# Kernel tuning notes

Hardware: AMD Instinct MI355X
Metric: run time of the kernel (lower is better)

Reference implementation:

```python
import jax, jax.numpy as jnp
import numpy as np

N = 50000
E = 1600000
IN_CH = 128
OUT_CH = 128
NEG_SLOPE = 0.2


def _gat_conv(x, W, att_src, att_dst, bias, src, dst, heads, out_ch, concat):
    # x: [N, F_in], W: [F_in, heads*out_ch], att_*: [heads, out_ch]
    n = x.shape[0]
    h = (x @ W).reshape(n, heads, out_ch)                    # [N, H, C]
    a_src = jnp.einsum('nhc,hc->nh', h, att_src)             # [N, H]
    a_dst = jnp.einsum('nhc,hc->nh', h, att_dst)             # [N, H]
    logits = jax.nn.leaky_relu(a_src[src] + a_dst[dst], NEG_SLOPE)  # [Etot, H]
    m = jax.ops.segment_max(logits, dst, num_segments=n)     # per-dst max (self-loops ensure non-empty)
    e = jnp.exp(logits - m[dst])
    denom = jax.ops.segment_sum(e, dst, num_segments=n)
    alpha = e / denom[dst]                                   # [Etot, H]
    msgs = h[src] * alpha[:, :, None]                        # [Etot, H, C]
    out = jax.ops.segment_sum(msgs, dst, num_segments=n)     # [N, H, C]
    out = out.reshape(n, heads * out_ch) if concat else out.mean(axis=1)
    return out + bias


def setup_inputs() -> dict:
    key = jax.random.key(0)
    ks = jax.random.split(key, 12)
    x = jax.random.normal(ks[0], (N, IN_CH), dtype=jnp.float32)
    edge_index = jax.random.randint(ks[1], (2, E), 0, N, dtype=jnp.int32)
    s = 0.1
    W_map = jax.random.normal(ks[2], (IN_CH, OUT_CH), dtype=jnp.float32) * s
    b_map = jnp.zeros((OUT_CH,), dtype=jnp.float32)
    # conv1: 128 -> 8 per head, 8 heads
    W1 = jax.random.normal(ks[3], (OUT_CH, 64), dtype=jnp.float32) * s
    att_src1 = jax.random.normal(ks[4], (8, 8), dtype=jnp.float32) * s
    att_dst1 = jax.random.normal(ks[5], (8, 8), dtype=jnp.float32) * s
    b1 = jnp.zeros((64,), dtype=jnp.float32)
    # conv2: 64 -> 128, 1 head, concat=False
    W2 = jax.random.normal(ks[6], (64, OUT_CH), dtype=jnp.float32) * s
    att_src2 = jax.random.normal(ks[7], (1, OUT_CH), dtype=jnp.float32) * s
    att_dst2 = jax.random.normal(ks[8], (1, OUT_CH), dtype=jnp.float32) * s
    b2 = jnp.zeros((OUT_CH,), dtype=jnp.float32)
    return {"x": x, "edge_index": edge_index, "W_map": W_map, "b_map": b_map,
            "W1": W1, "att_src1": att_src1, "att_dst1": att_dst1, "b1": b1,
            "W2": W2, "att_src2": att_src2, "att_dst2": att_dst2, "b2": b2}


def reference(x, edge_index, W_map, b_map, W1, att_src1, att_dst1, b1,
              W2, att_src2, att_dst2, b2):
    # add self-loops (PyG GATConv default)
    loops = jnp.arange(N, dtype=edge_index.dtype)
    src = jnp.concatenate([edge_index[0], loops])
    dst = jnp.concatenate([edge_index[1], loops])
    h = x @ W_map + b_map                                   # feature_mapping (dropout inactive in eval)
    h = _gat_conv(h, W1, att_src1, att_dst1, b1, src, dst, heads=8, out_ch=8, concat=True)
    h = jax.nn.elu(h)
    out = _gat_conv(h, W2, att_src2, att_dst2, b2, src, dst, heads=1, out_ch=OUT_CH, concat=False)
    return out
```

## Files before the change

### kernel.cpp

```cpp
#include <hip/hip_runtime.h>
#include <cstdint>
#include <cstddef>

#define NEG_SLOPE 0.2f
#define NBIN_MAX 1024
#define CAP_T 2560
#define SC_BLOCKS 512

typedef __attribute__((ext_vector_type(8))) short bf16x8;
typedef __attribute__((ext_vector_type(4))) float f32x4;

__device__ __forceinline__ float leaky(float x) { return x > 0.f ? x : NEG_SLOPE * x; }
__device__ __forceinline__ float blo(unsigned u) { return __uint_as_float(u << 16); }
__device__ __forceinline__ float bhi(unsigned u) { return __uint_as_float(u & 0xffff0000u); }
__device__ __forceinline__ unsigned short f2b(float f) {
    unsigned b = __float_as_uint(f);
    return (unsigned short)((b + 0x7fffu + ((b >> 16) & 1u)) >> 16);
}

__global__ void prep_kernel(const float* __restrict__ Wm, const float* __restrict__ W1,
                            const float* __restrict__ bm, const float* __restrict__ W2,
                            unsigned short* __restrict__ WcT, float* __restrict__ bc,
                            unsigned short* __restrict__ W2T, int* __restrict__ ccur,
                            int nbin) {
    int t = blockIdx.x * 256 + threadIdx.x;
    if (t < nbin) ccur[t] = 0;
    if (t < 8192) {
        int n = t >> 7, k = t & 127;
        float acc = 0.f;
        for (int c = 0; c < 128; c++) acc = fmaf(Wm[k * 128 + c], W1[c * 64 + n], acc);
        WcT[n * 128 + k] = f2b(acc);
        if (t < 64) {
            float a = 0.f;
            for (int c = 0; c < 128; c++) a = fmaf(bm[c], W1[c * 64 + t], a);
            bc[t] = a;
        }
    } else if (t < 16384) {
        int u = t - 8192;
        int n = u >> 6, k = u & 63;
        W2T[n * 64 + k] = f2b(W2[k * 128 + n]);
    }
}

__global__ __launch_bounds__(256) void phase2_kernel(
    const int* __restrict__ src, const int* __restrict__ dst, int E, int nbin,
    int* __restrict__ ccur, unsigned* __restrict__ tmp,
    const float* __restrict__ x, const unsigned short* __restrict__ WcT,
    const float* __restrict__ bc, const float* __restrict__ att_s,
    const float* __restrict__ att_d, unsigned short* __restrict__ h1b,
    float* __restrict__ as1, float* __restrict__ ad1, int N) {
    __shared__ int cnt[NBIN_MAX];
    if (blockIdx.x < SC_BLOCKS) {
        for (int i = threadIdx.x; i < nbin; i += 256) cnt[i] = 0;
        __syncthreads();
        int E4 = E >> 2;
        int chunk4 = (E4 + SC_BLOCKS - 1) / SC_BLOCKS;
        int b4 = blockIdx.x * chunk4;
        int e4 = b4 + chunk4; if (e4 > E4) e4 = E4;
        const int4* dst4 = (const int4*)dst;
        const int4* src4 = (const int4*)src;
        bool last = (blockIdx.x == SC_BLOCKS - 1);
        for (int i = b4 + threadIdx.x; i < e4; i += 256) {
            int4 d = dst4[i];
            atomicAdd(&cnt[d.x >> 6], 1);
            atomicAdd(&cnt[d.y >> 6], 1);
            atomicAdd(&cnt[d.z >> 6], 1);
            atomicAdd(&cnt[d.w >> 6], 1);
        }
        if (last)
            for (int i = (E4 << 2) + threadIdx.x; i < E; i += 256)
                atomicAdd(&cnt[dst[i] >> 6], 1);
        __syncthreads();
        for (int i = threadIdx.x; i < nbin; i += 256) {
            int c = cnt[i];
            cnt[i] = c ? atomicAdd(&ccur[i], c) : 0;
        }
        __syncthreads();
        for (int i = b4 + threadIdx.x; i < e4; i += 256) {
            int4 d = dst4[i];
            int4 s = src4[i];
#pragma unroll
            for (int k = 0; k < 4; k++) {
                int dd = (k == 0) ? d.x : (k == 1) ? d.y : (k == 2) ? d.z : d.w;
                int ss = (k == 0) ? s.x : (k == 1) ? s.y : (k == 2) ? s.z : s.w;
                int bin = dd >> 6;
                int p = atomicAdd(&cnt[bin], 1);
                if (p < CAP_T)
                    tmp[(size_t)bin * CAP_T + p] = ((unsigned)ss << 6) | (unsigned)(dd & 63);
            }
        }
        if (last)
            for (int i = (E4 << 2) + threadIdx.x; i < E; i += 256) {
                int dd = dst[i];
                int bin = dd >> 6;
                int p = atomicAdd(&cnt[bin], 1);
                if (p < CAP_T)
                    tmp[(size_t)bin * CAP_T + p] = ((unsigned)src[i] << 6) | (unsigned)(dd & 63);
            }
        return;
    }
    int wave = threadIdx.x >> 6, l = threadIdx.x & 63;
    int mtile = (blockIdx.x - SC_BLOCKS) * 4 + wave;
    int mtiles = N >> 4;
    if (mtile >= mtiles) return;
    int lm = l & 15, quad = l >> 4;
    const float* xr = x + ((size_t)(mtile * 16 + lm)) * 128 + quad * 8;
    f32x4 acc[4];
#pragma unroll
    for (int nt = 0; nt < 4; nt++) acc[nt] = (f32x4){0.f, 0.f, 0.f, 0.f};
#pragma unroll
    for (int kk = 0; kk < 4; kk++) {
        float4 xa = ((const float4*)(xr + kk * 32))[0];
        float4 xb = ((const float4*)(xr + kk * 32 + 4))[0];
        bf16x8 a;
        a[0] = (short)f2b(xa.x); a[1] = (short)f2b(xa.y);
        a[2] = (short)f2b(xa.z); a[3] = (short)f2b(xa.w);
        a[4] = (short)f2b(xb.x); a[5] = (short)f2b(xb.y);
        a[6] = (short)f2b(xb.z); a[7] = (short)f2b(xb.w);
#pragma unroll
        for (int nt = 0; nt < 4; nt++) {
            bf16x8 b = *(const bf16x8*)(WcT + (nt * 16 + lm) * 128 + kk * 32 + quad * 8);
            acc[nt] = __builtin_amdgcn_mfma_f32_16x16x32_bf16(a, b, acc[nt], 0, 0, 0);
        }
    }
    float vs[4][4], vd[4][4];
#pragma unroll
    for (int nt = 0; nt < 4; nt++) {
        int col = nt * 16 + lm;
        float sA = att_s[col], dA = att_d[col], bcv = bc[col];
#pragma unroll
        for (int r = 0; r < 4; r++) {
            float hv = acc[nt][r] + bcv;
            int row = mtile * 16 + quad * 4 + r;
            h1b[(size_t)row * 64 + col] = f2b(hv);
            vs[nt][r] = hv * sA;
            vd[nt][r] = hv * dA;
        }
    }
#pragma unroll
    for (int m = 1; m < 8; m <<= 1)
#pragma unroll
        for (int nt = 0; nt < 4; nt++)
#pragma unroll
            for (int r = 0; r < 4; r++) {
                vs[nt][r] += __shfl_xor(vs[nt][r], m);
                vd[nt][r] += __shfl_xor(vd[nt][r], m);
            }
    if ((lm & 7) == 0) {
        int hbase = lm >> 3;
#pragma unroll
        for (int nt = 0; nt < 4; nt++) {
            int H = 2 * nt + hbase;
#pragma unroll
            for (int r = 0; r < 4; r++) {
                int row = mtile * 16 + quad * 4 + r;
                as1[row * 8 + H] = vs[nt][r];
                ad1[row * 8 + H] = vd[nt][r];
            }
        }
    }
}

__global__ __launch_bounds__(256) void bin_finalize(
    const unsigned* __restrict__ tmp, const int* __restrict__ ccur,
    int* __restrict__ off, int* __restrict__ degv,
    unsigned short* __restrict__ bucket, int N) {
    __shared__ int cnt[64];
    __shared__ int cur[64];
    __shared__ unsigned short lbkt[CAP_T];
    int tid = threadIdx.x, b = blockIdx.x;
    if (tid < 64) cnt[tid] = 0;
    __syncthreads();
    int ecnt = ccur[b]; if (ecnt > CAP_T) ecnt = CAP_T;
    const unsigned* t = tmp + (size_t)b * CAP_T;
    const uint4* t4 = (const uint4*)t;
    int e4 = ecnt >> 2;
    for (int i = tid; i < e4; i += 256) {
        uint4 v = t4[i];
        atomicAdd(&cnt[v.x & 63u], 1);
        atomicAdd(&cnt[v.y & 63u], 1);
        atomicAdd(&cnt[v.z & 63u], 1);
        atomicAdd(&cnt[v.w & 63u], 1);
    }
    for (int i = (e4 << 2) + tid; i < ecnt; i += 256)
        atomicAdd(&cnt[t[i] & 63u], 1);
    __syncthreads();
    if (tid < 64) {
        int v = cnt[tid];
        int incl = v;
#pragma unroll
        for (int s = 1; s < 64; s <<= 1) {
            int u = __shfl_up(incl, s);
            if (tid >= s) incl += u;
        }
        int excl = incl - v;
        int node = b * 64 + tid;
        if (node < N) { off[node] = b * CAP_T + excl; degv[node] = v; }
        cur[tid] = excl;
    }
    __syncthreads();
    for (int i = tid; i < e4; i += 256) {
        uint4 v = t4[i];
        int p0 = atomicAdd(&cur[v.x & 63u], 1); lbkt[p0] = (unsigned short)(v.x >> 6);
        int p1 = atomicAdd(&cur[v.y & 63u], 1); lbkt[p1] = (unsigned short)(v.y >> 6);
        int p2 = atomicAdd(&cur[v.z & 63u], 1); lbkt[p2] = (unsigned short)(v.z >> 6);
        int p3 = atomicAdd(&cur[v.w & 63u], 1); lbkt[p3] = (unsigned short)(v.w >> 6);
    }
    for (int i = (e4 << 2) + tid; i < ecnt; i += 256) {
        unsigned u = t[i];
        int p = atomicAdd(&cur[u & 63u], 1);
        lbkt[p] = (unsigned short)(u >> 6);
    }
    __syncthreads();
    unsigned short* db = bucket + (size_t)b * CAP_T;
    int e8 = ecnt >> 3;
    uint4* d4 = (uint4*)db;
    const uint4* l4 = (const uint4*)lbkt;
    for (int i = tid; i < e8; i += 256) d4[i] = l4[i];
    for (int i = (e8 << 3) + tid; i < ecnt; i += 256) db[i] = lbkt[i];
}

__global__ __launch_bounds__(256) void conv1_agg(
    const int* __restrict__ off, const int* __restrict__ degv,
    const unsigned short* __restrict__ bucket,
    const unsigned* __restrict__ h1b, const float* __restrict__ as1,
    const float* __restrict__ ad1, const float* __restrict__ b1,
    unsigned* __restrict__ h1act, int N) {
    __shared__ uint2 lw[4][32][8];
    int wave = threadIdx.x >> 6, l = threadIdx.x & 63;
    int n = blockIdx.x * 4 + wave;
    if (n >= N) return;
    int begin = off[n];
    int deg = degv[n];
    int h = l & 7, eslot = l >> 3;
    float adst_h = ad1[n * 8 + h];
    float wself_h = __expf(leaky(as1[n * 8 + h] + adst_h));
    int c = l & 31, hp = c >> 2, half = l >> 5;
    float wself_c = __shfl(wself_h, hp);
    float acc0 = 0.f, acc1 = 0.f;
    if (half == 0) {
        unsigned u = h1b[(size_t)n * 32 + c];
        acc0 = wself_c * blo(u);
        acc1 = wself_c * bhi(u);
    }
    float den_l = 0.f;
    unsigned ps[4]; float pa[4];
#pragma unroll
    for (int k = 0; k < 4; k++) {
        int j = eslot + 8 * k;
        ps[k] = (j < deg) ? (unsigned)bucket[begin + j] : 0u;
    }
#pragma unroll
    for (int k = 0; k < 4; k++) pa[k] = as1[ps[k] * 8 + h];
    for (int c0 = 0; c0 < deg; c0 += 32) {
#pragma unroll
        for (int k = 0; k < 4; k++) {
            int e = eslot + 8 * k;
            float w = __expf(leaky(pa[k] + adst_h));
            if (c0 + e >= deg) w = 0.f;
            den_l += w;
            lw[wave][e][h] = make_uint2(__float_as_uint(w), ps[k]);
        }
        int c1 = c0 + 32;
        if (c1 < deg) {
#pragma unroll
            for (int k = 0; k < 4; k++) {
                int j = c1 + eslot + 8 * k;
                ps[k] = (j < deg) ? (unsigned)bucket[begin + j] : 0u;
            }
#pragma unroll
            for (int k = 0; k < 4; k++) pa[k] = as1[ps[k] * 8 + h];
        }
        int cend = deg - c0; if (cend > 32) cend = 32;
        int e = half;
        for (; e + 14 < cend; e += 16) {
            float w[8]; unsigned s[8], u[8];
#pragma unroll
            for (int k = 0; k < 8; k++) {
                uint2 p = lw[wave][e + 2 * k][hp];
                w[k] = __uint_as_float(p.x); s[k] = p.y;
            }
#pragma unroll
            for (int k = 0; k < 8; k++) u[k] = h1b[(size_t)s[k] * 32 + c];
#pragma unroll
            for (int k = 0; k < 8; k++) {
                acc0 = fmaf(w[k], blo(u[k]), acc0);
                acc1 = fmaf(w[k], bhi(u[k]), acc1);
            }
        }
        for (; e < cend; e += 2) {
            uint2 p = lw[wave][e][hp];
            unsigned u = h1b[(size_t)p.y * 32 + c];
            float w = __uint_as_float(p.x);
            acc0 = fmaf(w, blo(u), acc0);
            acc1 = fmaf(w, bhi(u), acc1);
        }
    }
    den_l += __shfl_xor(den_l, 8);
    den_l += __shfl_xor(den_l, 16);
    den_l += __shfl_xor(den_l, 32);
    float den_full = den_l + wself_h;
    float den_c = __shfl(den_full, hp);
    acc0 += __shfl_xor(acc0, 32);
    acc1 += __shfl_xor(acc1, 32);
    if (half == 0) {
        float inv = 1.f / den_c;
        float2 bb = ((const float2*)b1)[c];
        float o0 = acc0 * inv + bb.x;
        float o1 = acc1 * inv + bb.y;
        o0 = o0 > 0.f ? o0 : __expf(o0) - 1.f;
        o1 = o1 > 0.f ? o1 : __expf(o1) - 1.f;
        h1act[(size_t)n * 32 + c] = (unsigned)f2b(o0) | ((unsigned)f2b(o1) << 16);
    }
}

__global__ __launch_bounds__(256) void gemm2_mfma(
    const unsigned short* __restrict__ h1act, const unsigned short* __restrict__ W2T,
    const float* __restrict__ att_s2, const float* __restrict__ att_d2,
    unsigned short* __restrict__ h2b, float* __restrict__ as2, float* __restrict__ ad2,
    int N) {
    int wave = threadIdx.x >> 6, l = threadIdx.x & 63;
    int mtile = blockIdx.x * 4 + wave;
    int mtiles = N >> 4;
    if (mtile >= mtiles) return;
    int lm = l & 15, quad = l >> 4;
    const unsigned short* ar = h1act + (size_t)(mtile * 16 + lm) * 64 + quad * 8;
    bf16x8 a0 = *(const bf16x8*)(ar);
    bf16x8 a1 = *(const bf16x8*)(ar + 32);
    f32x4 acc[8];
#pragma unroll
    for (int nt = 0; nt < 8; nt++) acc[nt] = (f32x4){0.f, 0.f, 0.f, 0.f};
#pragma unroll
    for (int nt = 0; nt < 8; nt++) {
        const unsigned short* br = W2T + (nt * 16 + lm) * 64 + quad * 8;
        bf16x8 b0 = *(const bf16x8*)(br);
        bf16x8 b1v = *(const bf16x8*)(br + 32);
        acc[nt] = __builtin_amdgcn_mfma_f32_16x16x32_bf16(a0, b0, acc[nt], 0, 0, 0);
        acc[nt] = __builtin_amdgcn_mfma_f32_16x16x32_bf16(a1, b1v, acc[nt], 0, 0, 0);
    }
    float vs[4] = {0.f, 0.f, 0.f, 0.f}, vd[4] = {0.f, 0.f, 0.f, 0.f};
#pragma unroll
    for (int nt = 0; nt < 8; nt++) {
        int col = nt * 16 + lm;
        float sA = att_s2[col], dA = att_d2[col];
#pragma unroll
        for (int r = 0; r < 4; r++) {
            float hv = acc[nt][r];
            int row = mtile * 16 + quad * 4 + r;
            h2b[(size_t)row * 128 + col] = f2b(hv);
            vs[r] = fmaf(hv, sA, vs[r]);
            vd[r] = fmaf(hv, dA, vd[r]);
        }
    }
#pragma unroll
    for (int m = 1; m < 16; m <<= 1)
#pragma unroll
        for (int r = 0; r < 4; r++) {
            vs[r] += __shfl_xor(vs[r], m);
            vd[r] += __shfl_xor(vd[r], m);
        }
    if (lm == 0) {
#pragma unroll
        for (int r = 0; r < 4; r++) {
            int row = mtile * 16 + quad * 4 + r;
            as2[row] = vs[r];
            ad2[row] = vd[r];
        }
    }
}

__global__ __launch_bounds__(256) void conv2_agg(
    const int* __restrict__ off, const int* __restrict__ degv,
    const unsigned short* __restrict__ bucket,
    const unsigned* __restrict__ h2b, const float* __restrict__ as2,
    const float* __restrict__ ad2, const float* __restrict__ b2,
    float* __restrict__ out, int N) {
    __shared__ uint2 ew[4][64];
    int wave = threadIdx.x >> 6, l = threadIdx.x & 63;
    int n = blockIdx.x * 4 + wave;
    if (n >= N) return;
    int begin = off[n];
    int deg = degv[n];
    float adst = ad2[n];
    float wself = __expf(leaky(as2[n] + adst));
    unsigned us = h2b[(size_t)n * 64 + l];
    float acc0 = wself * blo(us);
    float acc1 = wself * bhi(us);
    float den_l = 0.f;
    for (int c0 = 0; c0 < deg; c0 += 64) {
        int j = c0 + l;
        float w = 0.f; unsigned s = 0;
        if (j < deg) {
            s = bucket[begin + j];
            w = __expf(leaky(as2[s] + adst));
        }
        den_l += w;
        ew[wave][l] = make_uint2(__float_as_uint(w), s);
        int cend = deg - c0; if (cend > 64) cend = 64;
        int jj = 0;
        for (; jj + 8 <= cend; jj += 8) {
            float w[8]; unsigned s8[8], u[8];
#pragma unroll
            for (int k = 0; k < 8; k++) {
                uint2 p = ew[wave][jj + k];
                w[k] = __uint_as_float(p.x); s8[k] = p.y;
            }
#pragma unroll
            for (int k = 0; k < 8; k++) u[k] = h2b[(size_t)s8[k] * 64 + l];
#pragma unroll
            for (int k = 0; k < 8; k++) {
                acc0 = fmaf(w[k], blo(u[k]), acc0);
                acc1 = fmaf(w[k], bhi(u[k]), acc1);
            }
        }
        for (; jj < cend; jj++) {
            uint2 p0 = ew[wave][jj];
            unsigned u0 = h2b[(size_t)p0.y * 64 + l];
            float w0 = __uint_as_float(p0.x);
            acc0 = fmaf(w0, blo(u0), acc0); acc1 = fmaf(w0, bhi(u0), acc1);
        }
    }
#pragma unroll
    for (int s = 1; s < 64; s <<= 1) den_l += __shfl_xor(den_l, s);
    float inv = 1.f / (den_l + wself);
    float2 bb = ((const float2*)b2)[l];
    ((float2*)out)[(size_t)n * 64 + l] =
        make_float2(acc0 * inv + bb.x, acc1 * inv + bb.y);
}

extern "C" void kernel_launch(void* const* d_in, const int* in_sizes, int n_in,
                              void* d_out, int out_size, void* d_ws, size_t ws_size,
                              hipStream_t stream) {
    const float* x   = (const float*)d_in[0];
    const int*   ei  = (const int*)d_in[1];
    const float* Wm  = (const float*)d_in[2];
    const float* bm  = (const float*)d_in[3];
    const float* W1  = (const float*)d_in[4];
    const float* As1 = (const float*)d_in[5];
    const float* Ad1 = (const float*)d_in[6];
    const float* b1  = (const float*)d_in[7];
    const float* W2  = (const float*)d_in[8];
    const float* As2 = (const float*)d_in[9];
    const float* Ad2 = (const float*)d_in[10];
    const float* b2  = (const float*)d_in[11];
    int N = in_sizes[0] / 128;
    int E = in_sizes[1] / 2;
    const int* srcv = ei;
    const int* dstv = ei + E;

    char* p = (char*)d_ws;
    auto alloc = [&](size_t bytes) {
        void* r = (void*)p;
        p += (bytes + 255) & ~(size_t)255;
        return r;
    };
    int nbin = (N + 63) / 64;
    int*   degv   = (int*)alloc((size_t)N * 4);
    int*   off    = (int*)alloc((size_t)N * 4);
    int*   ccur   = (int*)alloc((size_t)nbin * 4);
    unsigned short* bucket = (unsigned short*)alloc((size_t)nbin * CAP_T * 2);
    unsigned short* WcT  = (unsigned short*)alloc(64 * 128 * 2);
    float*          bc   = (float*)alloc(64 * 4);
    unsigned short* W2T  = (unsigned short*)alloc(128 * 64 * 2);
    unsigned short* h1b  = (unsigned short*)alloc((size_t)N * 64 * 2);
    float* a_s1   = (float*)alloc((size_t)N * 8 * 4);
    float* a_d1   = (float*)alloc((size_t)N * 8 * 4);
    unsigned* h1act = (unsigned*)alloc((size_t)N * 64 * 2);
    unsigned short* h2b = (unsigned short*)alloc((size_t)N * 128 * 2);
    unsigned* tmp = (unsigned*)h2b;
    float* a_s2   = (float*)alloc((size_t)N * 4);
    float* a_d2   = (float*)alloc((size_t)N * 4);
    float* outp   = (float*)d_out;

    int mtiles = N >> 4;
    int gemm_blocks = (mtiles + 3) / 4;
    prep_kernel<<<64, 256, 0, stream>>>(Wm, W1, bm, W2, WcT, bc, W2T, ccur, nbin);
    phase2_kernel<<<SC_BLOCKS + gemm_blocks, 256, 0, stream>>>(
        srcv, dstv, E, nbin, ccur, tmp, x, WcT, bc, As1, Ad1, h1b, a_s1, a_d1, N);
    bin_finalize<<<nbin, 256, 0, stream>>>(tmp, ccur, off, degv, bucket, N);
    conv1_agg<<<(N + 3) / 4, 256, 0, stream>>>(off, degv, bucket, (const unsigned*)h1b, a_s1, a_d1, b1, h1act, N);
    gemm2_mfma<<<(mtiles + 3) / 4, 256, 0, stream>>>((const unsigned short*)h1act, W2T, As2, Ad2, h2b, a_s2, a_d2, N);
    conv2_agg<<<(N + 3) / 4, 256, 0, stream>>>(off, degv, bucket, (const unsigned*)h2b, a_s2, a_d2, b2, outp, N);
}
```

Measured before the change: 270.5 us.

## Widen gathers to 8-byte loads and software-pipeline edge batches in both aggregations

Both aggregation kernels now gather 8 bytes per lane (four bf16 features) instead of 4, so each wave processes 4 (conv1) or 2 (conv2) edges at once. Edge chunks grow to 64 for conv1, and the inner loop is software-pipelined: the next batch of 8 gathers is issued before the current batch's FMAs. Neighbour offsets are pre-shifted into byte offsets in shared memory, and the shared array is padded to 9 columns to avoid bank conflicts. The unrolled full batches process padded zero-weight edges, which costs extra FMAs and loads for low-degree nodes, and the extra in-flight loads raise register pressure.

```diff
diff --git a/kernel.cpp b/kernel.cpp
--- a/kernel.cpp
+++ b/kernel.cpp
@@ -226,91 +226,115 @@
     const unsigned* __restrict__ h1b, const float* __restrict__ as1,
     const float* __restrict__ ad1, const float* __restrict__ b1,
     unsigned* __restrict__ h1act, int N) {
-    __shared__ uint2 lw[4][32][8];
+    __shared__ uint2 lw[4][64][9];
     int wave = threadIdx.x >> 6, l = threadIdx.x & 63;
     int n = blockIdx.x * 4 + wave;
     if (n >= N) return;
     int begin = off[n];
     int deg = degv[n];
     int h = l & 7, eslot = l >> 3;
+    int qq = l & 15, quarter = l >> 4, hh = qq >> 1;
+    unsigned qoff = (unsigned)(qq << 3);
+    const char* h1c = (const char*)h1b;
     float adst_h = ad1[n * 8 + h];
     float wself_h = __expf(leaky(as1[n * 8 + h] + adst_h));
-    int c = l & 31, hp = c >> 2, half = l >> 5;
-    float wself_c = __shfl(wself_h, hp);
-    float acc0 = 0.f, acc1 = 0.f;
-    if (half == 0) {
-        unsigned u = h1b[(size_t)n * 32 + c];
-        acc0 = wself_c * blo(u);
-        acc1 = wself_c * bhi(u);
+    float wself_c = __shfl(wself_h, hh);
+    float acc[4] = {0.f, 0.f, 0.f, 0.f};
+    if (quarter == 0) {
+        uint2 us = *(const uint2*)(h1c + ((unsigned)n << 7) + qoff);
+        acc[0] = wself_c * blo(us.x);
+        acc[1] = wself_c * bhi(us.x);
+        acc[2] = wself_c * blo(us.y);
+        acc[3] = wself_c * bhi(us.y);
     }
     float den_l = 0.f;
-    unsigned ps[4]; float pa[4];
-#pragma unroll
-    for (int k = 0; k < 4; k++) {
+    unsigned ps[8]; float pa[8];
+#pragma unroll
+    for (int k = 0; k < 8; k++) {
         int j = eslot + 8 * k;
         ps[k] = (j < deg) ? (unsigned)bucket[begin + j] : 0u;
     }
 #pragma unroll
-    for (int k = 0; k < 4; k++) pa[k] = as1[ps[k] * 8 + h];
-    for (int c0 = 0; c0 < deg; c0 += 32) {
-#pragma unroll
-        for (int k = 0; k < 4; k++) {
+    for (int k = 0; k < 8; k++) pa[k] = as1[ps[k] * 8 + h];
+    for (int c0 = 0; c0 < deg; c0 += 64) {
+#pragma unroll
+        for (int k = 0; k < 8; k++) {
             int e = eslot + 8 * k;
             float w = __expf(leaky(pa[k] + adst_h));
             if (c0 + e >= deg) w = 0.f;
             den_l += w;
-            lw[wave][e][h] = make_uint2(__float_as_uint(w), ps[k]);
-        }
-        int c1 = c0 + 32;
+            lw[wave][e][h] = make_uint2(__float_as_uint(w), ps[k] << 7);
+        }
+        int c1 = c0 + 64;
         if (c1 < deg) {
 #pragma unroll
-            for (int k = 0; k < 4; k++) {
+            for (int k = 0; k < 8; k++) {
                 int j = c1 + eslot + 8 * k;
                 ps[k] = (j < deg) ? (unsigned)bucket[begin + j] : 0u;
             }
 #pragma unroll
-            for (int k = 0; k < 4; k++) pa[k] = as1[ps[k] * 8 + h];
-        }
-        int cend = deg - c0; if (cend > 32) cend = 32;
-        int e = half;
-        for (; e + 14 < cend; e += 16) {
-            float w[8]; unsigned s[8], u[8];
+            for (int k = 0; k < 8; k++) pa[k] = as1[ps[k] * 8 + h];
+        }
+        int cend = deg - c0; if (cend > 64) cend = 64;
+        int K = (cend + 3) >> 2;
+        int nb = (K + 7) >> 3;
+        float wv[8]; uint2 u[8];
+#pragma unroll
+        for (int k = 0; k < 8; k++) {
+            uint2 p = lw[wave][4 * k + quarter][hh];
+            wv[k] = __uint_as_float(p.x);
+            u[k] = *(const uint2*)(h1c + p.y + qoff);
+        }
+        for (int b = 1; b < nb; b++) {
+            float wn[8]; uint2 un[8];
 #pragma unroll
             for (int k = 0; k < 8; k++) {
-                uint2 p = lw[wave][e + 2 * k][hp];
-                w[k] = __uint_as_float(p.x); s[k] = p.y;
-            }
-#pragma unroll
-            for (int k = 0; k < 8; k++) u[k] = h1b[(size_t)s[k] * 32 + c];
+                uint2 p = lw[wave][((b << 3) + k) * 4 + quarter][hh];
+                wn[k] = __uint_as_float(p.x);
+                un[k] = *(const uint2*)(h1c + p.y + qoff);
+            }
 #pragma unroll
             for (int k = 0; k < 8; k++) {
-                acc0 = fmaf(w[k], blo(u[k]), acc0);
-                acc1 = fmaf(w[k], bhi(u[k]), acc1);
-            }
-        }
-        for (; e < cend; e += 2) {
-            uint2 p = lw[wave][e][hp];
-            unsigned u = h1b[(size_t)p.y * 32 + c];
-            float w = __uint_as_float(p.x);
-            acc0 = fmaf(w, blo(u), acc0);
-            acc1 = fmaf(w, bhi(u), acc1);
+                acc[0] = fmaf(wv[k], blo(u[k].x), acc[0]);
+                acc[1] = fmaf(wv[k], bhi(u[k].x), acc[1]);
+                acc[2] = fmaf(wv[k], blo(u[k].y), acc[2]);
+                acc[3] = fmaf(wv[k], bhi(u[k].y), acc[3]);
+            }
+#pragma unroll
+            for (int k = 0; k < 8; k++) { wv[k] = wn[k]; u[k] = un[k]; }
+        }
+#pragma unroll
+        for (int k = 0; k < 8; k++) {
+            acc[0] = fmaf(wv[k], blo(u[k].x), acc[0]);
+            acc[1] = fmaf(wv[k], bhi(u[k].x), acc[1]);
+            acc[2] = fmaf(wv[k], blo(u[k].y), acc[2]);
+            acc[3] = fmaf(wv[k], bhi(u[k].y), acc[3]);
         }
     }
     den_l += __shfl_xor(den_l, 8);
     den_l += __shfl_xor(den_l, 16);
     den_l += __shfl_xor(den_l, 32);
     float den_full = den_l + wself_h;
-    float den_c = __shfl(den_full, hp);
-    acc0 += __shfl_xor(acc0, 32);
-    acc1 += __shfl_xor(acc1, 32);
-    if (half == 0) {
+    float den_c = __shfl(den_full, hh);
+#pragma unroll
+    for (int i = 0; i < 4; i++) {
+        acc[i] += __shfl_xor(acc[i], 16);
+        acc[i] += __shfl_xor(acc[i], 32);
+    }
+    if (quarter == 0) {
         float inv = 1.f / den_c;
-        float2 bb = ((const float2*)b1)[c];
-        float o0 = acc0 * inv + bb.x;
-        float o1 = acc1 * inv + bb.y;
+        float4 bb = ((const float4*)b1)[qq];
+        float o0 = acc[0] * inv + bb.x;
+        float o1 = acc[1] * inv + bb.y;
+        float o2 = acc[2] * inv + bb.z;
+        float o3 = acc[3] * inv + bb.w;
         o0 = o0 > 0.f ? o0 : __expf(o0) - 1.f;
         o1 = o1 > 0.f ? o1 : __expf(o1) - 1.f;
-        h1act[(size_t)n * 32 + c] = (unsigned)f2b(o0) | ((unsigned)f2b(o1) << 16);
+        o2 = o2 > 0.f ? o2 : __expf(o2) - 1.f;
+        o3 = o3 > 0.f ? o3 : __expf(o3) - 1.f;
+        ((uint2*)h1act)[(size_t)n * 16 + qq] = make_uint2(
+            (unsigned)f2b(o0) | ((unsigned)f2b(o1) << 16),
+            (unsigned)f2b(o2) | ((unsigned)f2b(o3) << 16));
     }
 }
 
@@ -381,51 +405,77 @@
     if (n >= N) return;
     int begin = off[n];
     int deg = degv[n];
+    int half = l >> 5, q = l & 31;
+    unsigned qoff = (unsigned)(q << 3);
+    const char* h2c = (const char*)h2b;
     float adst = ad2[n];
     float wself = __expf(leaky(as2[n] + adst));
-    unsigned us = h2b[(size_t)n * 64 + l];
-    float acc0 = wself * blo(us);
-    float acc1 = wself * bhi(us);
+    float acc[4] = {0.f, 0.f, 0.f, 0.f};
+    if (half == 0) {
+        uint2 us = *(const uint2*)(h2c + ((unsigned)n << 8) + qoff);
+        acc[0] = wself * blo(us.x);
+        acc[1] = wself * bhi(us.x);
+        acc[2] = wself * blo(us.y);
+        acc[3] = wself * bhi(us.y);
+    }
     float den_l = 0.f;
     for (int c0 = 0; c0 < deg; c0 += 64) {
         int j = c0 + l;
-        float w = 0.f; unsigned s = 0;
+        float w = 0.f; unsigned soff = 0u;
         if (j < deg) {
-            s = bucket[begin + j];
+            unsigned s = (unsigned)bucket[begin + j];
+            soff = s << 8;
             w = __expf(leaky(as2[s] + adst));
         }
         den_l += w;
-        ew[wave][l] = make_uint2(__float_as_uint(w), s);
+        ew[wave][l] = make_uint2(__float_as_uint(w), soff);
         int cend = deg - c0; if (cend > 64) cend = 64;
-        int jj = 0;
-        for (; jj + 8 <= cend; jj += 8) {
-            float w[8]; unsigned s8[8], u[8];
+        int K = (cend + 1) >> 1;
+        int nb = (K + 7) >> 3;
+        float wv[8]; uint2 u[8];
+#pragma unroll
+        for (int k = 0; k < 8; k++) {
+            uint2 p = ew[wave][2 * k + half];
+            wv[k] = __uint_as_float(p.x);
+            u[k] = *(const uint2*)(h2c + p.y + qoff);
+        }
+        for (int b = 1; b < nb; b++) {
+            float wn[8]; uint2 un[8];
 #pragma unroll
             for (int k = 0; k < 8; k++) {
-                uint2 p = ew[wave][jj + k];
-                w[k] = __uint_as_float(p.x); s8[k] = p.y;
-            }
-#pragma unroll
-            for (int k = 0; k < 8; k++) u[k] = h2b[(size_t)s8[k] * 64 + l];
+                uint2 p = ew[wave][((b << 3) + k) * 2 + half];
+                wn[k] = __uint_as_float(p.x);
+                un[k] = *(const uint2*)(h2c + p.y + qoff);
+            }
 #pragma unroll
             for (int k = 0; k < 8; k++) {
-                acc0 = fmaf(w[k], blo(u[k]), acc0);
-                acc1 = fmaf(w[k], bhi(u[k]), acc1);
-            }
-        }
-        for (; jj < cend; jj++) {
-            uint2 p0 = ew[wave][jj];
-            unsigned u0 = h2b[(size_t)p0.y * 64 + l];
-            float w0 = __uint_as_float(p0.x);
-            acc0 = fmaf(w0, blo(u0), acc0); acc1 = fmaf(w0, bhi(u0), acc1);
+                acc[0] = fmaf(wv[k], blo(u[k].x), acc[0]);
+                acc[1] = fmaf(wv[k], bhi(u[k].x), acc[1]);
+                acc[2] = fmaf(wv[k], blo(u[k].y), acc[2]);
+                acc[3] = fmaf(wv[k], bhi(u[k].y), acc[3]);
+            }
+#pragma unroll
+            for (int k = 0; k < 8; k++) { wv[k] = wn[k]; u[k] = un[k]; }
+        }
+#pragma unroll
+        for (int k = 0; k < 8; k++) {
+            acc[0] = fmaf(wv[k], blo(u[k].x), acc[0]);
+            acc[1] = fmaf(wv[k], bhi(u[k].x), acc[1]);
+            acc[2] = fmaf(wv[k], blo(u[k].y), acc[2]);
+            acc[3] = fmaf(wv[k], bhi(u[k].y), acc[3]);
         }
     }
 #pragma unroll
     for (int s = 1; s < 64; s <<= 1) den_l += __shfl_xor(den_l, s);
     float inv = 1.f / (den_l + wself);
-    float2 bb = ((const float2*)b2)[l];
-    ((float2*)out)[(size_t)n * 64 + l] =
-        make_float2(acc0 * inv + bb.x, acc1 * inv + bb.y);
+#pragma unroll
+    for (int i = 0; i < 4; i++) acc[i] += __shfl_xor(acc[i], 32);
+    if (half == 0) {
+        float4 bb = ((const float4*)b2)[q];
+        ((float4*)out)[(size_t)n * 32 + q] = make_float4(
+            acc[0] * inv + bb.x, acc[1] * inv + bb.y,
+            acc[2] * inv + bb.z, acc[3] * inv + bb.w);
+    }
 }
 
 extern "C" void kernel_launch(void* const* d_in, const int* in_sizes, int n_in,
```

Measured after the change: 293.7 us. +8.6%, slower.

## Gather neighbor rows with 16-byte vector loads in both GAT aggregation kernels

Applied to the files above, without the earlier changes.

Both aggregation kernels now have each lane own 8 contiguous bf16 channels and gather them with a single 16-byte load per edge. The wave processes several edges at once, and per-edge weights are computed in registers. Neighbor indices and attention scores are prefetched one chunk ahead, which removes the shared-memory weight/index staging. The goal is fewer, wider gather instructions and more memory-level parallelism. The cost is more registers and a cross-lane reduction of 8 accumulators at the end.

```diff
diff --git a/kernel.cpp b/kernel.cpp
--- a/kernel.cpp
+++ b/kernel.cpp
@@ -226,91 +226,115 @@
     const unsigned* __restrict__ h1b, const float* __restrict__ as1,
     const float* __restrict__ ad1, const float* __restrict__ b1,
     unsigned* __restrict__ h1act, int N) {
-    __shared__ uint2 lw[4][32][8];
     int wave = threadIdx.x >> 6, l = threadIdx.x & 63;
     int n = blockIdx.x * 4 + wave;
     if (n >= N) return;
     int begin = off[n];
     int deg = degv[n];
-    int h = l & 7, eslot = l >> 3;
-    float adst_h = ad1[n * 8 + h];
-    float wself_h = __expf(leaky(as1[n * 8 + h] + adst_h));
-    int c = l & 31, hp = c >> 2, half = l >> 5;
-    float wself_c = __shfl(wself_h, hp);
-    float acc0 = 0.f, acc1 = 0.f;
-    if (half == 0) {
-        unsigned u = h1b[(size_t)n * 32 + c];
-        acc0 = wself_c * blo(u);
-        acc1 = wself_c * bhi(u);
+    int oo = l & 7, octet = l >> 3;
+    unsigned qoff = (unsigned)(oo << 4);
+    const char* h1c = (const char*)h1b;
+    float adst = ad1[n * 8 + oo];
+    float wself = __expf(leaky(as1[n * 8 + oo] + adst));
+    float acc[8] = {0.f, 0.f, 0.f, 0.f, 0.f, 0.f, 0.f, 0.f};
+    if (octet == 0) {
+        uint4 us = *(const uint4*)(h1c + ((size_t)n << 7) + qoff);
+        acc[0] = wself * blo(us.x); acc[1] = wself * bhi(us.x);
+        acc[2] = wself * blo(us.y); acc[3] = wself * bhi(us.y);
+        acc[4] = wself * blo(us.z); acc[5] = wself * bhi(us.z);
+        acc[6] = wself * blo(us.w); acc[7] = wself * bhi(us.w);
     }
     float den_l = 0.f;
-    unsigned ps[4]; float pa[4];
-#pragma unroll
-    for (int k = 0; k < 4; k++) {
-        int j = eslot + 8 * k;
-        ps[k] = (j < deg) ? (unsigned)bucket[begin + j] : 0u;
-    }
-#pragma unroll
-    for (int k = 0; k < 4; k++) pa[k] = as1[ps[k] * 8 + h];
-    for (int c0 = 0; c0 < deg; c0 += 32) {
-#pragma unroll
-        for (int k = 0; k < 4; k++) {
-            int e = eslot + 8 * k;
-            float w = __expf(leaky(pa[k] + adst_h));
-            if (c0 + e >= deg) w = 0.f;
-            den_l += w;
-            lw[wave][e][h] = make_uint2(__float_as_uint(w), ps[k]);
-        }
-        int c1 = c0 + 32;
-        if (c1 < deg) {
-#pragma unroll
-            for (int k = 0; k < 4; k++) {
-                int j = c1 + eslot + 8 * k;
-                ps[k] = (j < deg) ? (unsigned)bucket[begin + j] : 0u;
-            }
-#pragma unroll
-            for (int k = 0; k < 4; k++) pa[k] = as1[ps[k] * 8 + h];
-        }
-        int cend = deg - c0; if (cend > 32) cend = 32;
-        int e = half;
-        for (; e + 14 < cend; e += 16) {
-            float w[8]; unsigned s[8], u[8];
-#pragma unroll
-            for (int k = 0; k < 8; k++) {
-                uint2 p = lw[wave][e + 2 * k][hp];
-                w[k] = __uint_as_float(p.x); s[k] = p.y;
-            }
-#pragma unroll
-            for (int k = 0; k < 8; k++) u[k] = h1b[(size_t)s[k] * 32 + c];
-#pragma unroll
-            for (int k = 0; k < 8; k++) {
-                acc0 = fmaf(w[k], blo(u[k]), acc0);
-                acc1 = fmaf(w[k], bhi(u[k]), acc1);
-            }
-        }
-        for (; e < cend; e += 2) {
-            uint2 p = lw[wave][e][hp];
-            unsigned u = h1b[(size_t)p.y * 32 + c];
-            float w = __uint_as_float(p.x);
-            acc0 = fmaf(w, blo(u), acc0);
-            acc1 = fmaf(w, bhi(u), acc1);
+    unsigned sv[8]; float av[8];
+#pragma unroll
+    for (int j = 0; j < 8; j++) {
+        int e = 8 * j + octet;
+        sv[j] = (e < deg) ? (unsigned)bucket[begin + e] : 0u;
+    }
+#pragma unroll
+    for (int j = 0; j < 8; j++) {
+        float t = as1[sv[j] * 8 + oo];
+        av[j] = (8 * j + octet < deg) ? t : -1e30f;
+    }
+    for (int c0 = 0; c0 < deg; c0 += 64) {
+        uint4 uv[8];
+#pragma unroll
+        for (int j = 0; j < 8; j++) {
+            uv[j] = make_uint4(0u, 0u, 0u, 0u);
+            if (av[j] > -1e29f)
+                uv[j] = *(const uint4*)(h1c + ((size_t)sv[j] << 7) + qoff);
+        }
+        int c1 = c0 + 64;
+        bool more = c1 < deg;
+        unsigned sn[8];
+        if (more) {
+#pragma unroll
+            for (int j = 0; j < 8; j++) {
+                int e = c1 + 8 * j + octet;
+                sn[j] = (e < deg) ? (unsigned)bucket[begin + e] : 0u;
+            }
+        }
+        float wv[8];
+#pragma unroll
+        for (int j = 0; j < 8; j++) {
+            float w = __expf(leaky(av[j] + adst));
+            wv[j] = w; den_l += w;
+        }
+        if (more) {
+#pragma unroll
+            for (int j = 0; j < 8; j++) {
+                float t = as1[sn[j] * 8 + oo];
+                av[j] = (c1 + 8 * j + octet < deg) ? t : -1e30f;
+                sv[j] = sn[j];
+            }
+        }
+#pragma unroll
+        for (int j = 0; j < 8; j++) {
+            acc[0] = fmaf(wv[j], blo(uv[j].x), acc[0]);
+            acc[1] = fmaf(wv[j], bhi(uv[j].x), acc[1]);
+            acc[2] = fmaf(wv[j], blo(uv[j].y), acc[2]);
+            acc[3] = fmaf(wv[j], bhi(uv[j].y), acc[3]);
+            acc[4] = fmaf(wv[j], blo(uv[j].z), acc[4]);
+            acc[5] = fmaf(wv[j], bhi(uv[j].z), acc[5]);
+            acc[6] = fmaf(wv[j], blo(uv[j].w), acc[6]);
+            acc[7] = fmaf(wv[j], bhi(uv[j].w), acc[7]);
         }
     }
     den_l += __shfl_xor(den_l, 8);
     den_l += __shfl_xor(den_l, 16);
     den_l += __shfl_xor(den_l, 32);
-    float den_full = den_l + wself_h;
-    float den_c = __shfl(den_full, hp);
-    acc0 += __shfl_xor(acc0, 32);
-    acc1 += __shfl_xor(acc1, 32);
-    if (half == 0) {
-        float inv = 1.f / den_c;
-        float2 bb = ((const float2*)b1)[c];
-        float o0 = acc0 * inv + bb.x;
-        float o1 = acc1 * inv + bb.y;
+    float den = den_l + wself;
+#pragma unroll
+    for (int i = 0; i < 8; i++) {
+        acc[i] += __shfl_xor(acc[i], 8);
+        acc[i] += __shfl_xor(acc[i], 16);
+        acc[i] += __shfl_xor(acc[i], 32);
+    }
+    if (octet == 0) {
+        float inv = 1.f / den;
+        float4 b0 = ((const float4*)b1)[oo * 2];
+        float4 b1v = ((const float4*)b1)[oo * 2 + 1];
+        float o0 = acc[0] * inv + b0.x;
+        float o1 = acc[1] * inv + b0.y;
+        float o2 = acc[2] * inv + b0.z;
+        float o3 = acc[3] * inv + b0.w;
+        float o4 = acc[4] * inv + b1v.x;
+        float o5 = acc[5] * inv + b1v.y;
+        float o6 = acc[6] * inv + b1v.z;
+        float o7 = acc[7] * inv + b1v.w;
         o0 = o0 > 0.f ? o0 : __expf(o0) - 1.f;
         o1 = o1 > 0.f ? o1 : __expf(o1) - 1.f;
-        h1act[(size_t)n * 32 + c] = (unsigned)f2b(o0) | ((unsigned)f2b(o1) << 16);
+        o2 = o2 > 0.f ? o2 : __expf(o2) - 1.f;
+        o3 = o3 > 0.f ? o3 : __expf(o3) - 1.f;
+        o4 = o4 > 0.f ? o4 : __expf(o4) - 1.f;
+        o5 = o5 > 0.f ? o5 : __expf(o5) - 1.f;
+        o6 = o6 > 0.f ? o6 : __expf(o6) - 1.f;
+        o7 = o7 > 0.f ? o7 : __expf(o7) - 1.f;
+        unsigned r0 = (unsigned)f2b(o0) | ((unsigned)f2b(o1) << 16);
+        unsigned r1 = (unsigned)f2b(o2) | ((unsigned)f2b(o3) << 16);
+        unsigned r2 = (unsigned)f2b(o4) | ((unsigned)f2b(o5) << 16);
+        unsigned r3 = (unsigned)f2b(o6) | ((unsigned)f2b(o7) << 16);
+        ((uint4*)h1act)[(size_t)n * 8 + oo] = make_uint4(r0, r1, r2, r3);
     }
 }
 
@@ -375,57 +399,99 @@
     const unsigned* __restrict__ h2b, const float* __restrict__ as2,
     const float* __restrict__ ad2, const float* __restrict__ b2,
     float* __restrict__ out, int N) {
-    __shared__ uint2 ew[4][64];
     int wave = threadIdx.x >> 6, l = threadIdx.x & 63;
     int n = blockIdx.x * 4 + wave;
     if (n >= N) return;
     int begin = off[n];
     int deg = degv[n];
+    int qq = l & 15, quarter = l >> 4;
+    unsigned qoff = (unsigned)(qq << 4);
+    const char* h2c = (const char*)h2b;
     float adst = ad2[n];
     float wself = __expf(leaky(as2[n] + adst));
-    unsigned us = h2b[(size_t)n * 64 + l];
-    float acc0 = wself * blo(us);
-    float acc1 = wself * bhi(us);
+    float acc[8] = {0.f, 0.f, 0.f, 0.f, 0.f, 0.f, 0.f, 0.f};
+    if (quarter == 0) {
+        uint4 us = *(const uint4*)(h2c + ((size_t)n << 8) + qoff);
+        acc[0] = wself * blo(us.x); acc[1] = wself * bhi(us.x);
+        acc[2] = wself * blo(us.y); acc[3] = wself * bhi(us.y);
+        acc[4] = wself * blo(us.z); acc[5] = wself * bhi(us.z);
+        acc[6] = wself * blo(us.w); acc[7] = wself * bhi(us.w);
+    }
     float den_l = 0.f;
-    for (int c0 = 0; c0 < deg; c0 += 64) {
-        int j = c0 + l;
-        float w = 0.f; unsigned s = 0;
-        if (j < deg) {
-            s = bucket[begin + j];
-            w = __expf(leaky(as2[s] + adst));
-        }
-        den_l += w;
-        ew[wave][l] = make_uint2(__float_as_uint(w), s);
-        int cend = deg - c0; if (cend > 64) cend = 64;
-        int jj = 0;
-        for (; jj + 8 <= cend; jj += 8) {
-            float w[8]; unsigned s8[8], u[8];
-#pragma unroll
-            for (int k = 0; k < 8; k++) {
-                uint2 p = ew[wave][jj + k];
-                w[k] = __uint_as_float(p.x); s8[k] = p.y;
-            }
-#pragma unroll
-            for (int k = 0; k < 8; k++) u[k] = h2b[(size_t)s8[k] * 64 + l];
-#pragma unroll
-            for (int k = 0; k < 8; k++) {
-                acc0 = fmaf(w[k], blo(u[k]), acc0);
-                acc1 = fmaf(w[k], bhi(u[k]), acc1);
-            }
-        }
-        for (; jj < cend; jj++) {
-            uint2 p0 = ew[wave][jj];
-            unsigned u0 = h2b[(size_t)p0.y * 64 + l];
-            float w0 = __uint_as_float(p0.x);
-            acc0 = fmaf(w0, blo(u0), acc0); acc1 = fmaf(w0, bhi(u0), acc1);
-        }
-    }
-#pragma unroll
-    for (int s = 1; s < 64; s <<= 1) den_l += __shfl_xor(den_l, s);
-    float inv = 1.f / (den_l + wself);
-    float2 bb = ((const float2*)b2)[l];
-    ((float2*)out)[(size_t)n * 64 + l] =
-        make_float2(acc0 * inv + bb.x, acc1 * inv + bb.y);
+    unsigned sv[8]; float av[8];
+#pragma unroll
+    for (int j = 0; j < 8; j++) {
+        int e = 4 * j + quarter;
+        sv[j] = (e < deg) ? (unsigned)bucket[begin + e] : 0u;
+    }
+#pragma unroll
+    for (int j = 0; j < 8; j++) {
+        float t = as2[sv[j]];
+        av[j] = (4 * j + quarter < deg) ? t : -1e30f;
+    }
+    for (int c0 = 0; c0 < deg; c0 += 32) {
+        uint4 uv[8];
+#pragma unroll
+        for (int j = 0; j < 8; j++) {
+            uv[j] = make_uint4(0u, 0u, 0u, 0u);
+            if (av[j] > -1e29f)
+                uv[j] = *(const uint4*)(h2c + ((size_t)sv[j] << 8) + qoff);
+        }
+        int c1 = c0 + 32;
+        bool more = c1 < deg;
+        unsigned sn[8];
+        if (more) {
+#pragma unroll
+            for (int j = 0; j < 8; j++) {
+                int e = c1 + 4 * j + quarter;
+                sn[j] = (e < deg) ? (unsigned)bucket[begin + e] : 0u;
+            }
+        }
+        float wv[8];
+#pragma unroll
+        for (int j = 0; j < 8; j++) {
+            float w = __expf(leaky(av[j] + adst));
+            wv[j] = w; den_l += w;
+        }
+        if (more) {
+#pragma unroll
+            for (int j = 0; j < 8; j++) {
+                float t = as2[sn[j]];
+                av[j] = (c1 + 4 * j + quarter < deg) ? t : -1e30f;
+                sv[j] = sn[j];
+            }
+        }
+#pragma unroll
+        for (int j = 0; j < 8; j++) {
+            acc[0] = fmaf(wv[j], blo(uv[j].x), acc[0]);
+            acc[1] = fmaf(wv[j], bhi(uv[j].x), acc[1]);
+            acc[2] = fmaf(wv[j], blo(uv[j].y), acc[2]);
+            acc[3] = fmaf(wv[j], bhi(uv[j].y), acc[3]);
+            acc[4] = fmaf(wv[j], blo(uv[j].z), acc[4]);
+            acc[5] = fmaf(wv[j], bhi(uv[j].z), acc[5]);
+            acc[6] = fmaf(wv[j], blo(uv[j].w), acc[6]);
+            acc[7] = fmaf(wv[j], bhi(uv[j].w), acc[7]);
+        }
+    }
+    den_l += __shfl_xor(den_l, 16);
+    den_l += __shfl_xor(den_l, 32);
+    float den = den_l + wself;
+#pragma unroll
+    for (int i = 0; i < 8; i++) {
+        acc[i] += __shfl_xor(acc[i], 16);
+        acc[i] += __shfl_xor(acc[i], 32);
+    }
+    if (quarter == 0) {
+        float inv = 1.f / den;
+        float4 b0 = ((const float4*)b2)[qq * 2];
+        float4 b1v = ((const float4*)b2)[qq * 2 + 1];
+        ((float4*)out)[(size_t)n * 32 + qq * 2] = make_float4(
+            acc[0] * inv + b0.x, acc[1] * inv + b0.y,
+            acc[2] * inv + b0.z, acc[3] * inv + b0.w);
+        ((float4*)out)[(size_t)n * 32 + qq * 2 + 1] = make_float4(
+            acc[4] * inv + b1v.x, acc[5] * inv + b1v.y,
+            acc[6] * inv + b1v.z, acc[7] * inv + b1v.w);
+    }
 }
 
 extern "C" void kernel_launch(void* const* d_in, const int* in_sizes, int n_in,
```

New measurement: 277.8 us. +2.7%, slower.
